# Performance work log

Hardware: AMD Instinct MI355X
Metric: run time of the kernel (lower is better)

## Reference

```python
import jax, jax.numpy as jnp
import numpy as np

D_MODEL = 1024
EXPAND = 2
D_INNER = D_MODEL * EXPAND  # 2048
D_STATE = 16
D_CONV = 4
DT_RANK = (D_MODEL + 15) // 16  # 64
BATCH = 2
SEQ = 1024


def setup_inputs() -> dict:
    key = jax.random.key(0)
    ks = jax.random.split(key, 10)
    s = lambda d: 1.0 / np.sqrt(d)
    x = jax.random.normal(ks[0], (BATCH, SEQ, D_MODEL), dtype=jnp.float32)
    W_in = jax.random.normal(ks[1], (D_MODEL, 2 * D_INNER), dtype=jnp.float32) * s(D_MODEL)
    conv_w = jax.random.normal(ks[2], (D_INNER, D_CONV), dtype=jnp.float32) * s(D_CONV)
    conv_b = jax.random.normal(ks[3], (D_INNER,), dtype=jnp.float32) * 0.02
    W_x = jax.random.normal(ks[4], (D_INNER, DT_RANK + 2 * D_STATE), dtype=jnp.float32) * s(D_INNER)
    W_dt = jax.random.normal(ks[5], (DT_RANK, D_INNER), dtype=jnp.float32) * s(DT_RANK)
    b_dt = jax.random.uniform(ks[6], (D_INNER,), dtype=jnp.float32, minval=-4.0, maxval=-2.0)
    # S4D-real init: A = -[1..d_state] per channel
    A_log = jnp.log(jnp.tile(jnp.arange(1, D_STATE + 1, dtype=jnp.float32), (D_INNER, 1)))
    D = jnp.ones((D_INNER,), dtype=jnp.float32)
    W_out = jax.random.normal(ks[7], (D_INNER, D_MODEL), dtype=jnp.float32) * s(D_INNER)
    return {"x": x, "W_in": W_in, "conv_w": conv_w, "conv_b": conv_b,
            "W_x": W_x, "W_dt": W_dt, "b_dt": b_dt, "A_log": A_log,
            "D": D, "W_out": W_out}


def _mamba_forward(x, W_in, conv_w, conv_b, W_x, W_dt, b_dt, A_log, D, W_out):
    B, L, _ = x.shape
    # input projection -> [B, L, 2*d_inner], split into u (conv branch) and z (gate)
    xz = jnp.einsum('bld,de->ble', x, W_in)
    u, z = jnp.split(xz, 2, axis=-1)  # each [B, L, d_inner]

    # causal depthwise conv over time
    u_c = jnp.transpose(u, (0, 2, 1))                      # [B, d_inner, L]
    u_c = jnp.pad(u_c, ((0, 0), (0, 0), (D_CONV - 1, 0)))  # left pad for causality
    kern = conv_w[:, None, :]                              # [d_inner, 1, d_conv]
    u_c = jax.lax.conv_general_dilated(
        u_c, kern, window_strides=(1,), padding='VALID',
        dimension_numbers=('NCH', 'OIH', 'NCH'),
        feature_group_count=D_INNER)
    u_c = u_c + conv_b[None, :, None]
    u_c = jax.nn.silu(jnp.transpose(u_c, (0, 2, 1)))       # [B, L, d_inner]

    # data-dependent SSM parameters
    x_dbl = jnp.einsum('bld,de->ble', u_c, W_x)            # [B, L, dt_rank+2*d_state]
    dt_lowrank = x_dbl[..., :DT_RANK]
    Bmat = x_dbl[..., DT_RANK:DT_RANK + D_STATE]           # [B, L, d_state]
    Cmat = x_dbl[..., DT_RANK + D_STATE:]                  # [B, L, d_state]
    dt = jax.nn.softplus(jnp.einsum('blr,rd->bld', dt_lowrank, W_dt) + b_dt)

    A = -jnp.exp(A_log)                                    # [d_inner, d_state]

    # selective scan over time: h' = exp(dt*A) h + dt*B*u ; y = <h, C>
    def step(h, inp):
        u_t, dt_t, B_t, C_t = inp                          # [B,d], [B,d], [B,n], [B,n]
        dA = jnp.exp(dt_t[..., None] * A)                  # [B, d_inner, d_state]
        dBu = (dt_t * u_t)[..., None] * B_t[:, None, :]    # [B, d_inner, d_state]
        h = dA * h + dBu
        y_t = jnp.einsum('bdn,bn->bd', h, C_t)
        return h, y_t

    h0 = jnp.zeros((B, D_INNER, D_STATE), dtype=x.dtype)
    seq = (jnp.swapaxes(u_c, 0, 1), jnp.swapaxes(dt, 0, 1),
           jnp.swapaxes(Bmat, 0, 1), jnp.swapaxes(Cmat, 0, 1))
    _, ys = jax.lax.scan(step, h0, seq)                    # ys: [L, B, d_inner]
    y = jnp.swapaxes(ys, 0, 1) + u_c * D                   # skip term
    y = y * jax.nn.silu(z)                                 # gate
    return jnp.einsum('bld,de->ble', y, W_out)             # [B, L, d_model]


def reference(x, W_in, conv_w, conv_b, W_x, W_dt, b_dt, A_log, D, W_out):
    return _mamba_forward(x, W_in, conv_w, conv_b, W_x, W_dt, b_dt, A_log, D, W_out)
```

## Files before the change

kernel.cpp:

```cpp
#include <hip/hip_runtime.h>
#include <hip/hip_bf16.h>


typedef __attribute__((ext_vector_type(8))) short bfrag;
typedef __attribute__((ext_vector_type(4))) float f32x4;

#define CF   32
#define CLEN 32

__device__ __forceinline__ unsigned short f2bf(float f) {
    unsigned int u = __float_as_uint(f);
    u += 0x7FFF + ((u >> 16) & 1);
    return (unsigned short)(u >> 16);
}
__device__ __forceinline__ float bf2f(unsigned short s) {
    return __uint_as_float((unsigned int)s << 16);
}

__device__ __forceinline__ void async_copy16(const unsigned short* g,
                                             unsigned short* l) {
    __builtin_amdgcn_global_load_lds(
        (const __attribute__((address_space(1))) void*)g,
        (__attribute__((address_space(3))) void*)l, 16, 0, 0);
}

template<int MT, int NT>
__global__ __launch_bounds__(256) void gemm_bf16_v2(
    const unsigned short* __restrict__ A,
    const unsigned short* __restrict__ BT,
    float* __restrict__ C,
    unsigned short* __restrict__ Cb0,
    unsigned short* __restrict__ Cb1,
    int K, int lda, int ldb, int ldc, int split,
    const float* __restrict__ bias)
{
    constexpr int FI  = MT / 32;
    constexpr int FJ  = NT / 32;
    constexpr int ACH = MT / 32;
    constexpr int BCH = NT / 32;
    __shared__ __align__(16) unsigned short sA[MT * 64];
    __shared__ __align__(16) unsigned short sB[NT * 64];

    const int tid  = threadIdx.x;
    const int wave = tid >> 6, lane = tid & 63;
    const int lm   = lane & 15;
    const int quad = lane >> 4;
    const int wrow = (wave >> 1) * (MT / 2);
    const int wcol = (wave & 1) * (NT / 2);
    const int bm = blockIdx.y * MT, bn = blockIdx.x * NT;

    const int lrow = lane >> 3;
    const int lkb  = (lane & 7) ^ lrow;

    f32x4 acc[FI][FJ];
    #pragma unroll
    for (int i = 0; i < FI; ++i)
        #pragma unroll
        for (int j = 0; j < FJ; ++j) {
            acc[i][j][0] = 0.f; acc[i][j][1] = 0.f;
            acc[i][j][2] = 0.f; acc[i][j][3] = 0.f;
        }

    for (int k0 = 0; k0 < K; k0 += 64) {
        #pragma unroll
        for (int c = 0; c < ACH; ++c) {
            const int chunk = wave * ACH + c;
            const int row = chunk * 8 + lrow;
            async_copy16(&A[(size_t)(bm + row) * lda + k0 + lkb * 8],
                         &sA[chunk * 512 + lane * 8]);
        }
        #pragma unroll
        for (int c = 0; c < BCH; ++c) {
            const int chunk = wave * BCH + c;
            const int row = chunk * 8 + lrow;
            async_copy16(&BT[(size_t)(bn + row) * ldb + k0 + lkb * 8],
                         &sB[chunk * 512 + lane * 8]);
        }
        __syncthreads();

        #pragma unroll
        for (int ks = 0; ks < 2; ++ks) {
            bfrag af[FI], bf[FJ];
            #pragma unroll
            for (int i = 0; i < FI; ++i) {
                const int row = wrow + i * 16 + lm;
                const int slot = (ks * 4 + quad) ^ (row & 7);
                af[i] = *(const bfrag*)&sA[row * 64 + slot * 8];
            }
            #pragma unroll
            for (int j = 0; j < FJ; ++j) {
                const int row = wcol + j * 16 + lm;
                const int slot = (ks * 4 + quad) ^ (row & 7);
                bf[j] = *(const bfrag*)&sB[row * 64 + slot * 8];
            }
            #pragma unroll
            for (int i = 0; i < FI; ++i)
                #pragma unroll
                for (int j = 0; j < FJ; ++j)
                    acc[i][j] = __builtin_amdgcn_mfma_f32_16x16x32_bf16(
                        af[i], bf[j], acc[i][j], 0, 0, 0);
        }
        __syncthreads();
    }

    #pragma unroll
    for (int i = 0; i < FI; ++i)
        #pragma unroll
        for (int j = 0; j < FJ; ++j) {
            const int col = bn + wcol + j * 16 + lm;
            #pragma unroll
            for (int r = 0; r < 4; ++r) {
                const int row = bm + wrow + i * 16 + quad * 4 + r;
                float v = acc[i][j][r];
                if (bias != nullptr) {
                    v += bias[col];
                    v = (v > 20.f) ? v : logf(1.f + expf(v));
                    Cb0[(size_t)row * ldc + col] = f2bf(v);
                } else if (split > 0) {
                    if (col < split) Cb0[(size_t)row * split + col] = f2bf(v);
                    else             Cb1[(size_t)row * split + (col - split)] = f2bf(v);
                } else {
                    C[(size_t)row * ldc + col] = v;
                }
            }
        }
}

__global__ __launch_bounds__(256) void prep_fused(
    const float* __restrict__ W_in, const float* __restrict__ W_out,
    const float* __restrict__ W_dt, const float* __restrict__ x,
    unsigned short* __restrict__ wbT, unsigned short* __restrict__ wobT,
    unsigned short* __restrict__ wdtT, unsigned short* __restrict__ xb)
{
    __shared__ float tile[32][33];
    const int bx = blockIdx.x;
    const int tid = threadIdx.x;

    const float* in; unsigned short* out; int rows, cols, jt, it;
    if (bx < 4096)      { in = W_in;  out = wbT;  rows = 1024; cols = 4096;
                          jt = bx & 127; it = bx >> 7; }
    else if (bx < 6144) { int t = bx - 4096; in = W_out; out = wobT;
                          rows = 2048; cols = 1024; jt = t & 31; it = t >> 5; }
    else if (bx < 6272) { int t = bx - 6144; in = W_dt;  out = wdtT;
                          rows = 64;   cols = 2048; jt = t & 63; it = t >> 6; }
    else {
        int i = ((bx - 6272) * 256 + tid) * 4;
        float4 v = *(const float4*)&x[i];
        ushort4 o;
        o.x = f2bf(v.x); o.y = f2bf(v.y); o.z = f2bf(v.z); o.w = f2bf(v.w);
        *(ushort4*)&xb[i] = o;
        return;
    }
    const int j0 = jt * 32, i0 = it * 32;
    const int tx = tid & 31, ty = tid >> 5;
    #pragma unroll
    for (int k = 0; k < 4; ++k)
        tile[ty + 8 * k][tx] = in[(size_t)(i0 + ty + 8 * k) * cols + j0 + tx];
    __syncthreads();
    #pragma unroll
    for (int k = 0; k < 4; ++k)
        out[(size_t)(j0 + ty + 8 * k) * rows + i0 + tx] = f2bf(tile[tx][ty + 8 * k]);
}

#define SK_KS 128
__global__ __launch_bounds__(256) void gemm_f32_splitk(
    const unsigned short* __restrict__ A,
    const float* __restrict__ B,
    float* __restrict__ part)
{
    __shared__ __align__(16) float As[16][64];
    __shared__ __align__(16) float Bs[16][96];

    const int tid = threadIdx.x;
    const int mtile = blockIdx.x >> 4;
    const int kslice = blockIdx.x & 15;
    const int bm = mtile * 64;
    const int kbase = kslice * SK_KS;

    const int am = tid >> 2;
    const int ak = (tid & 3) << 2;

    const int ty = tid >> 4, tx = tid & 15;
    const int rm = ty << 2;
    const int rn = tx * 6;

    float acc[4][6] = {};

    for (int k0 = 0; k0 < SK_KS; k0 += 16) {
        ushort4 av = *(const ushort4*)&A[(size_t)(bm + am) * 2048 + kbase + k0 + ak];
        As[ak + 0][am] = bf2f(av.x);
        As[ak + 1][am] = bf2f(av.y);
        As[ak + 2][am] = bf2f(av.z);
        As[ak + 3][am] = bf2f(av.w);
        for (int i = tid; i < 384; i += 256) {
            int br = i / 24, bc = (i % 24) << 2;
            *(float4*)&Bs[br][bc] = *(const float4*)&B[(size_t)(kbase + k0 + br) * 96 + bc];
        }
        __syncthreads();

        #pragma unroll
        for (int k = 0; k < 16; ++k) {
            float4 a = *(const float4*)&As[k][rm];
            float b[6];
            #pragma unroll
            for (int j = 0; j < 6; ++j) b[j] = Bs[k][rn + j];
            #pragma unroll
            for (int j = 0; j < 6; ++j) {
                acc[0][j] += a.x * b[j];
                acc[1][j] += a.y * b[j];
                acc[2][j] += a.z * b[j];
                acc[3][j] += a.w * b[j];
            }
        }
        __syncthreads();
    }

    float* pout = part + (size_t)kslice * 196608;
    #pragma unroll
    for (int i = 0; i < 4; ++i) {
        float* crow = pout + (size_t)(bm + rm + i) * 96 + rn;
        #pragma unroll
        for (int j = 0; j < 6; ++j)
            crow[j] = acc[i][j];
    }
}

__global__ __launch_bounds__(256) void reduce_splitk(
    const float* __restrict__ part, float* __restrict__ xdbl,
    unsigned short* __restrict__ dtl)
{
    int i = (blockIdx.x * 256 + threadIdx.x) * 4;
    float4 acc = {0.f, 0.f, 0.f, 0.f};
    #pragma unroll
    for (int s = 0; s < 16; ++s) {
        float4 v = *(const float4*)&part[(size_t)s * 196608 + i];
        acc.x += v.x; acc.y += v.y; acc.z += v.z; acc.w += v.w;
    }
    *(float4*)&xdbl[i] = acc;
    int row = i / 96, col = i % 96;
    if (col < 64) {
        ushort4 o;
        o.x = f2bf(acc.x); o.y = f2bf(acc.y);
        o.z = f2bf(acc.z); o.w = f2bf(acc.w);
        *(ushort4*)&dtl[(size_t)row * 64 + col] = o;
    }
}

__global__ __launch_bounds__(256) void conv_silu_kernel(
    const unsigned short* __restrict__ ub, const float* __restrict__ cw,
    const float* __restrict__ cb, unsigned short* __restrict__ uc)
{
    int idx = blockIdx.x * 256 + threadIdx.x;
    int d = idx & 2047;
    int r = idx >> 11;
    int l = r & 1023;

    float4 w4 = *(const float4*)(cw + 4 * d);
    float w[4] = { w4.x, w4.y, w4.z, w4.w };
    float acc = cb[d];
    const unsigned short* up = ub + (size_t)r * 2048 + d;
    if (l >= 3) {
        acc += w[0] * bf2f(up[-3 * 2048]) + w[1] * bf2f(up[-2 * 2048])
             + w[2] * bf2f(up[-1 * 2048]) + w[3] * bf2f(up[0]);
    } else {
        #pragma unroll
        for (int j = 0; j < 4; ++j) {
            int lj = l - 3 + j;
            if (lj >= 0) acc += w[j] * bf2f(up[(j - 3) * 2048]);
        }
    }
    float sig = 1.f / (1.f + expf(-acc));
    uc[idx] = f2bf(acc * sig);
}

__global__ __launch_bounds__(256) void scan_pass1(
    const unsigned short* __restrict__ uc,
    const unsigned short* __restrict__ dtb,
    const float* __restrict__ xdbl,
    const float* __restrict__ A_log,
    float* __restrict__ Hend,
    float* __restrict__ Sdt)
{
    __shared__ __align__(16) unsigned short su [CLEN][256];
    __shared__ __align__(16) unsigned short sdt[CLEN][256];
    __shared__ float sB[CLEN][16];
    const int tid = threadIdx.x;
    const int bx  = blockIdx.x;
    const int c   = bx & (CF - 1);
    const int g   = (bx >> 5) & 7;
    const int b   = bx >> 8;
    const int dbase = g * 256;
    const int d   = dbase + tid;
    const size_t rowbase = (size_t)b * 1024 + c * CLEN;

    #pragma unroll
    for (int q = 0; q < 4; ++q) {
        int i = q * 256 + tid;
        int row = i >> 5, off = (i & 31) * 8;
        size_t gaddr = (rowbase + row) * 2048 + dbase + off;
        *(float4*)&su [row][off] = *(const float4*)&uc [gaddr];
        *(float4*)&sdt[row][off] = *(const float4*)&dtb[gaddr];
    }
    for (int i = tid; i < CLEN * 16; i += 256) {
        int tt = i >> 4, nn = i & 15;
        sB[tt][nn] = xdbl[(rowbase + tt) * 96 + 64 + nn];
    }

    float A2[16];
    {
        float al[16];
        #pragma unroll
        for (int q = 0; q < 4; ++q)
            *(float4*)&al[4 * q] = *(const float4*)&A_log[(size_t)d * 16 + 4 * q];
        #pragma unroll
        for (int n = 0; n < 16; ++n) A2[n] = -expf(al[n]) * 1.44269504f;
    }
    __syncthreads();

    float h[16];
    #pragma unroll
    for (int n = 0; n < 16; ++n) h[n] = 0.f;
    float sdtv = 0.f;

    #pragma unroll 4
    for (int t = 0; t < CLEN; ++t) {
        float dtv = bf2f(sdt[t][tid]);
        float uv  = bf2f(su [t][tid]);
        sdtv += dtv;
        float dtu = dtv * uv;
        float bl[16];
        #pragma unroll
        for (int q = 0; q < 4; ++q)
            *(float4*)&bl[4 * q] = *(const float4*)&sB[t][4 * q];
        #pragma unroll
        for (int n = 0; n < 16; ++n)
            h[n] = exp2f(dtv * A2[n]) * h[n] + dtu * bl[n];
    }

    size_t base = ((size_t)(b * CF + c) * 2048 + d) * 16;
    #pragma unroll
    for (int q = 0; q < 4; ++q)
        *(float4*)&Hend[base + 4 * q] = *(float4*)&h[4 * q];
    Sdt[(size_t)(b * CF + c) * 2048 + d] = sdtv;
}

__global__ __launch_bounds__(256) void scan_pass2(
    const float* __restrict__ Hend, const float* __restrict__ Sdt,
    const float* __restrict__ A_log, float* __restrict__ Hin)
{
    int gid = blockIdx.x * 256 + threadIdx.x;
    int b = gid >> 15;
    int rest = gid & 32767;
    int d = rest >> 4;
    float A2 = -expf(A_log[rest]) * 1.44269504f;
    float H = 0.f;
    #pragma unroll
    for (int c = 0; c < CF; ++c) {
        size_t sidx = (size_t)(b * CF + c) * 2048 + d;
        size_t idx  = ((size_t)(b * CF + c) << 15) + rest;
        Hin[idx] = H;
        H = exp2f(A2 * Sdt[sidx]) * H + Hend[idx];
    }
}

__global__ __launch_bounds__(256) void scan_pass3(
    const unsigned short* __restrict__ uc,
    const unsigned short* __restrict__ dtb,
    const unsigned short* __restrict__ zb,
    const float* __restrict__ xdbl,
    const float* __restrict__ A_log,
    const float* __restrict__ Dvec,
    const float* __restrict__ Hin,
    unsigned short* __restrict__ yb)
{
    __shared__ __align__(16) unsigned short su [CLEN][256];
    __shared__ __align__(16) unsigned short sdt[CLEN][256];
    __shared__ __align__(16) unsigned short sz [CLEN][256];
    __shared__ float sBC[CLEN][32];
    const int tid = threadIdx.x;
    const int bx  = blockIdx.x;
    const int c   = bx & (CF - 1);
    const int g   = (bx >> 5) & 7;
    const int b   = bx >> 8;
    const int dbase = g * 256;
    const int d   = dbase + tid;
    const size_t rowbase = (size_t)b * 1024 + c * CLEN;

    #pragma unroll
    for (int q = 0; q < 4; ++q) {
        int i = q * 256 + tid;
        int row = i >> 5, off = (i & 31) * 8;
        size_t gaddr = (rowbase + row) * 2048 + dbase + off;
        *(float4*)&su [row][off] = *(const float4*)&uc [gaddr];
        *(float4*)&sdt[row][off] = *(const float4*)&dtb[gaddr];
        *(float4*)&sz [row][off] = *(const float4*)&zb [gaddr];
    }
    for (int i = tid; i < CLEN * 32; i += 256) {
        int tt = i >> 5, j = i & 31;
        sBC[tt][j] = xdbl[(rowbase + tt) * 96 + 64 + j];
    }

    float A2[16];
    {
        float al[16];
        #pragma unroll
        for (int q = 0; q < 4; ++q)
            *(float4*)&al[4 * q] = *(const float4*)&A_log[(size_t)d * 16 + 4 * q];
        #pragma unroll
        for (int n = 0; n < 16; ++n) A2[n] = -expf(al[n]) * 1.44269504f;
    }
    const float Dd = Dvec[d];

    float h[16];
    {
        size_t base = ((size_t)(b * CF + c) * 2048 + d) * 16;
        #pragma unroll
        for (int q = 0; q < 4; ++q)
            *(float4*)&h[4 * q] = *(const float4*)&Hin[base + 4 * q];
    }
    __syncthreads();

    #pragma unroll 4
    for (int t = 0; t < CLEN; ++t) {
        float dtv = bf2f(sdt[t][tid]);
        float uv  = bf2f(su [t][tid]);
        float zv  = bf2f(sz [t][tid]);
        float dtu = dtv * uv;
        float bl[16], cl[16];
        #pragma unroll
        for (int q = 0; q < 4; ++q) {
            *(float4*)&bl[4 * q] = *(const float4*)&sBC[t][4 * q];
            *(float4*)&cl[4 * q] = *(const float4*)&sBC[t][16 + 4 * q];
        }
        float acc = uv * Dd;
        #pragma unroll
        for (int n = 0; n < 16; ++n) {
            h[n] = exp2f(dtv * A2[n]) * h[n] + dtu * bl[n];
            acc += h[n] * cl[n];
        }
        float yv = acc * zv / (1.f + expf(-zv));
        sz[t][tid] = f2bf(yv);
    }
    __syncthreads();

    #pragma unroll
    for (int q = 0; q < 4; ++q) {
        int i = q * 256 + tid;
        int row = i >> 5, off = (i & 31) * 8;
        size_t gaddr = (rowbase + row) * 2048 + dbase + off;
        *(float4*)&yb[gaddr] = *(const float4*)&sz[row][off];
    }
}

extern "C" void kernel_launch(void* const* d_in, const int* in_sizes, int n_in,
                              void* d_out, int out_size, void* d_ws, size_t ws_size,
                              hipStream_t stream)
{
    const float* x      = (const float*)d_in[0];
    const float* W_in   = (const float*)d_in[1];
    const float* conv_w = (const float*)d_in[2];
    const float* conv_b = (const float*)d_in[3];
    const float* W_x    = (const float*)d_in[4];
    const float* W_dt   = (const float*)d_in[5];
    const float* b_dt   = (const float*)d_in[6];
    const float* A_log  = (const float*)d_in[7];
    const float* Dv     = (const float*)d_in[8];
    const float* W_out  = (const float*)d_in[9];
    float* out = (float*)d_out;

    float* ws = (float*)d_ws;
    unsigned short* ub  = (unsigned short*)ws;
    unsigned short* dtb = ub;
    unsigned short* uc  = ub + 4194304;
    float* xdbl = ws + 4194304;
    unsigned short* dtl = (unsigned short*)(xdbl + 196608);
    float* Hend = xdbl + 196608 + 65536;
    float* Hin  = Hend + 2097152;
    float* Sdt  = Hin + 2097152;
    float* part = Hend;
    unsigned short* zb   = (unsigned short*)(Sdt + 131072);
    unsigned short* xb   = zb + 4194304;
    unsigned short* wbT  = xb + 2097152;
    unsigned short* wobT = wbT + 4194304;
    unsigned short* wdtT = wobT + 2097152;
    unsigned short* yb   = wbT;

    dim3 blk(256);

    prep_fused<<<8320, blk, 0, stream>>>(W_in, W_out, W_dt, x,
                                         wbT, wobT, wdtT, xb);

    gemm_bf16_v2<128, 128><<<dim3(32, 16), blk, 0, stream>>>(
        xb, wbT, nullptr, ub, zb, 1024, 1024, 1024, 2048, 2048, nullptr);

    conv_silu_kernel<<<(2048 * 2048) / 256, blk, 0, stream>>>(ub, conv_w, conv_b, uc);

    gemm_f32_splitk<<<512, blk, 0, stream>>>(uc, W_x, part);
    reduce_splitk<<<192, blk, 0, stream>>>(part, xdbl, dtl);

    gemm_bf16_v2<128, 128><<<dim3(16, 16), blk, 0, stream>>>(
        dtl, wdtT, nullptr, dtb, nullptr, 64, 64, 64, 2048, 0, b_dt);

    scan_pass1<<<512, blk, 0, stream>>>(uc, dtb, xdbl, A_log, Hend, Sdt);
    scan_pass2<<<256, blk, 0, stream>>>(Hend, Sdt, A_log, Hin);
    scan_pass3<<<512, blk, 0, stream>>>(uc, dtb, zb, xdbl, A_log, Dv, Hin, yb);

    gemm_bf16_v2<64, 64><<<dim3(16, 32), blk, 0, stream>>>(
        yb, wobT, out, nullptr, nullptr, 2048, 2048, 2048, 1024, 0, nullptr);
}
```

Baseline: 269.4 us.

## Fuse dt projection and softplus into scan passes; vectorize conv-silu

Removes the standalone dt GEMM (K=64) and its 8 MB bf16 dt buffer. Each scan block now computes its own 32x256 dt tile with MFMA from the low-rank dtl and the transposed W_dt, applies bias and softplus, and writes the result to shared memory. Because pass1 and pass3 each do this, the dt GEMM runs twice, but one launch and a full write plus two reads of dt are saved. The conv-silu kernel also now handles 8 channels per thread with vector loads and stores.

```diff
diff --git a/kernel.cpp b/kernel.cpp
--- a/kernel.cpp
+++ b/kernel.cpp
@@ -31,8 +31,7 @@
     float* __restrict__ C,
     unsigned short* __restrict__ Cb0,
     unsigned short* __restrict__ Cb1,
-    int K, int lda, int ldb, int ldc, int split,
-    const float* __restrict__ bias)
+    int K, int lda, int ldb, int ldc, int split)
 {
     constexpr int FI  = MT / 32;
     constexpr int FJ  = NT / 32;
@@ -112,11 +111,7 @@
             for (int r = 0; r < 4; ++r) {
                 const int row = bm + wrow + i * 16 + quad * 4 + r;
                 float v = acc[i][j][r];
-                if (bias != nullptr) {
-                    v += bias[col];
-                    v = (v > 20.f) ? v : logf(1.f + expf(v));
-                    Cb0[(size_t)row * ldc + col] = f2bf(v);
-                } else if (split > 0) {
+                if (split > 0) {
                     if (col < split) Cb0[(size_t)row * split + col] = f2bf(v);
                     else             Cb1[(size_t)row * split + (col - split)] = f2bf(v);
                 } else {
@@ -251,38 +246,112 @@
     const float* __restrict__ cb, unsigned short* __restrict__ uc)
 {
     int idx = blockIdx.x * 256 + threadIdx.x;
-    int d = idx & 2047;
-    int r = idx >> 11;
-    int l = r & 1023;
-
-    float4 w4 = *(const float4*)(cw + 4 * d);
-    float w[4] = { w4.x, w4.y, w4.z, w4.w };
-    float acc = cb[d];
-    const unsigned short* up = ub + (size_t)r * 2048 + d;
-    if (l >= 3) {
-        acc += w[0] * bf2f(up[-3 * 2048]) + w[1] * bf2f(up[-2 * 2048])
-             + w[2] * bf2f(up[-1 * 2048]) + w[3] * bf2f(up[0]);
-    } else {
+    int r  = idx >> 8;
+    int d0 = (idx & 255) * 8;
+    int l  = r & 1023;
+
+    float4 w[8];
+    #pragma unroll
+    for (int q = 0; q < 8; ++q) w[q] = *(const float4*)&cw[(d0 + q) * 4];
+
+    float acc[8];
+    #pragma unroll
+    for (int q = 0; q < 8; ++q) acc[q] = cb[d0 + q];
+
+    const unsigned short* up = ub + (size_t)r * 2048 + d0;
+    #pragma unroll
+    for (int j = 0; j < 4; ++j) {
+        int lj = l - 3 + j;
+        if (lj >= 0) {
+            const unsigned short* rp = up + (ptrdiff_t)(j - 3) * 2048;
+            ushort4 a = *(const ushort4*)&rp[0];
+            ushort4 b4 = *(const ushort4*)&rp[4];
+            float uv[8] = { bf2f(a.x), bf2f(a.y), bf2f(a.z), bf2f(a.w),
+                            bf2f(b4.x), bf2f(b4.y), bf2f(b4.z), bf2f(b4.w) };
+            #pragma unroll
+            for (int q = 0; q < 8; ++q)
+                acc[q] += uv[q] * ((const float*)&w[q])[j];
+        }
+    }
+    ushort4 o0, o1;
+    float s;
+    s = 1.f / (1.f + expf(-acc[0])); o0.x = f2bf(acc[0] * s);
+    s = 1.f / (1.f + expf(-acc[1])); o0.y = f2bf(acc[1] * s);
+    s = 1.f / (1.f + expf(-acc[2])); o0.z = f2bf(acc[2] * s);
+    s = 1.f / (1.f + expf(-acc[3])); o0.w = f2bf(acc[3] * s);
+    s = 1.f / (1.f + expf(-acc[4])); o1.x = f2bf(acc[4] * s);
+    s = 1.f / (1.f + expf(-acc[5])); o1.y = f2bf(acc[5] * s);
+    s = 1.f / (1.f + expf(-acc[6])); o1.z = f2bf(acc[6] * s);
+    s = 1.f / (1.f + expf(-acc[7])); o1.w = f2bf(acc[7] * s);
+    *(ushort4*)&uc[(size_t)r * 2048 + d0]     = o0;
+    *(ushort4*)&uc[(size_t)r * 2048 + d0 + 4] = o1;
+}
+
+__device__ __forceinline__ void compute_dt_tile(
+    const unsigned short* __restrict__ wdtT, const float* __restrict__ b_dt,
+    const unsigned short (*sdtl)[72], unsigned short (*sdt)[256],
+    int dbase, int tid)
+{
+    const int wave = tid >> 6, lane = tid & 63;
+    const int lm = lane & 15, quad = lane >> 4;
+
+    f32x4 dacc[2][4];
+    #pragma unroll
+    for (int mi = 0; mi < 2; ++mi)
         #pragma unroll
         for (int j = 0; j < 4; ++j) {
-            int lj = l - 3 + j;
-            if (lj >= 0) acc += w[j] * bf2f(up[(j - 3) * 2048]);
-        }
-    }
-    float sig = 1.f / (1.f + expf(-acc));
-    uc[idx] = f2bf(acc * sig);
+            dacc[mi][j][0] = 0.f; dacc[mi][j][1] = 0.f;
+            dacc[mi][j][2] = 0.f; dacc[mi][j][3] = 0.f;
+        }
+
+    #pragma unroll
+    for (int kc = 0; kc < 2; ++kc) {
+        bfrag a[2], bw[4];
+        #pragma unroll
+        for (int mi = 0; mi < 2; ++mi)
+            a[mi] = *(const bfrag*)&sdtl[mi * 16 + lm][kc * 32 + quad * 8];
+        #pragma unroll
+        for (int j = 0; j < 4; ++j) {
+            const int dg = dbase + wave * 64 + j * 16 + lm;
+            bw[j] = *(const bfrag*)&wdtT[(size_t)dg * 64 + kc * 32 + quad * 8];
+        }
+        #pragma unroll
+        for (int mi = 0; mi < 2; ++mi)
+            #pragma unroll
+            for (int j = 0; j < 4; ++j)
+                dacc[mi][j] = __builtin_amdgcn_mfma_f32_16x16x32_bf16(
+                    a[mi], bw[j], dacc[mi][j], 0, 0, 0);
+    }
+
+    #pragma unroll
+    for (int j = 0; j < 4; ++j) {
+        const int dl = wave * 64 + j * 16 + lm;
+        const float bb = b_dt[dbase + dl];
+        #pragma unroll
+        for (int mi = 0; mi < 2; ++mi)
+            #pragma unroll
+            for (int r = 0; r < 4; ++r) {
+                const int t = mi * 16 + quad * 4 + r;
+                float v = dacc[mi][j][r] + bb;
+                v = (v > 20.f) ? v : logf(1.f + expf(v));
+                sdt[t][dl] = f2bf(v);
+            }
+    }
 }
 
 __global__ __launch_bounds__(256) void scan_pass1(
     const unsigned short* __restrict__ uc,
-    const unsigned short* __restrict__ dtb,
+    const unsigned short* __restrict__ dtl,
+    const unsigned short* __restrict__ wdtT,
+    const float* __restrict__ b_dt,
     const float* __restrict__ xdbl,
     const float* __restrict__ A_log,
     float* __restrict__ Hend,
     float* __restrict__ Sdt)
 {
-    __shared__ __align__(16) unsigned short su [CLEN][256];
-    __shared__ __align__(16) unsigned short sdt[CLEN][256];
+    __shared__ __align__(16) unsigned short su  [CLEN][256];
+    __shared__ __align__(16) unsigned short sdt [CLEN][256];
+    __shared__ __align__(16) unsigned short sdtl[CLEN][72];
     __shared__ float sB[CLEN][16];
     const int tid = threadIdx.x;
     const int bx  = blockIdx.x;
@@ -297,9 +366,13 @@
     for (int q = 0; q < 4; ++q) {
         int i = q * 256 + tid;
         int row = i >> 5, off = (i & 31) * 8;
-        size_t gaddr = (rowbase + row) * 2048 + dbase + off;
-        *(float4*)&su [row][off] = *(const float4*)&uc [gaddr];
-        *(float4*)&sdt[row][off] = *(const float4*)&dtb[gaddr];
+        *(float4*)&su[row][off] = *(const float4*)&uc[(rowbase + row) * 2048 + dbase + off];
+    }
+    #pragma unroll
+    for (int q = 0; q < 2; ++q) {
+        int i = q * 256 + tid;
+        int row = i >> 4, col = (i & 15) * 4;
+        *(ushort4*)&sdtl[row][col] = *(const ushort4*)&dtl[(rowbase + row) * 64 + col];
     }
     for (int i = tid; i < CLEN * 16; i += 256) {
         int tt = i >> 4, nn = i & 15;
@@ -315,6 +388,9 @@
         #pragma unroll
         for (int n = 0; n < 16; ++n) A2[n] = -expf(al[n]) * 1.44269504f;
     }
+    __syncthreads();
+
+    compute_dt_tile(wdtT, b_dt, sdtl, sdt, dbase, tid);
     __syncthreads();
 
     float h[16];
@@ -365,7 +441,9 @@
 
 __global__ __launch_bounds__(256) void scan_pass3(
     const unsigned short* __restrict__ uc,
-    const unsigned short* __restrict__ dtb,
+    const unsigned short* __restrict__ dtl,
+    const unsigned short* __restrict__ wdtT,
+    const float* __restrict__ b_dt,
     const unsigned short* __restrict__ zb,
     const float* __restrict__ xdbl,
     const float* __restrict__ A_log,
@@ -373,9 +451,10 @@
     const float* __restrict__ Hin,
     unsigned short* __restrict__ yb)
 {
-    __shared__ __align__(16) unsigned short su [CLEN][256];
-    __shared__ __align__(16) unsigned short sdt[CLEN][256];
-    __shared__ __align__(16) unsigned short sz [CLEN][256];
+    __shared__ __align__(16) unsigned short su  [CLEN][256];
+    __shared__ __align__(16) unsigned short sdt [CLEN][256];
+    __shared__ __align__(16) unsigned short sz  [CLEN][256];
+    __shared__ __align__(16) unsigned short sdtl[CLEN][72];
     __shared__ float sBC[CLEN][32];
     const int tid = threadIdx.x;
     const int bx  = blockIdx.x;
@@ -391,9 +470,14 @@
         int i = q * 256 + tid;
         int row = i >> 5, off = (i & 31) * 8;
         size_t gaddr = (rowbase + row) * 2048 + dbase + off;
-        *(float4*)&su [row][off] = *(const float4*)&uc [gaddr];
-        *(float4*)&sdt[row][off] = *(const float4*)&dtb[gaddr];
-        *(float4*)&sz [row][off] = *(const float4*)&zb [gaddr];
+        *(float4*)&su[row][off] = *(const float4*)&uc[gaddr];
+        *(float4*)&sz[row][off] = *(const float4*)&zb[gaddr];
+    }
+    #pragma unroll
+    for (int q = 0; q < 2; ++q) {
+        int i = q * 256 + tid;
+        int row = i >> 4, col = (i & 15) * 4;
+        *(ushort4*)&sdtl[row][col] = *(const ushort4*)&dtl[(rowbase + row) * 64 + col];
     }
     for (int i = tid; i < CLEN * 32; i += 256) {
         int tt = i >> 5, j = i & 31;
@@ -418,6 +502,9 @@
         for (int q = 0; q < 4; ++q)
             *(float4*)&h[4 * q] = *(const float4*)&Hin[base + 4 * q];
     }
+    __syncthreads();
+
+    compute_dt_tile(wdtT, b_dt, sdtl, sdt, dbase, tid);
     __syncthreads();
 
     #pragma unroll 4
@@ -470,7 +557,6 @@
 
     float* ws = (float*)d_ws;
     unsigned short* ub  = (unsigned short*)ws;
-    unsigned short* dtb = ub;
     unsigned short* uc  = ub + 4194304;
     float* xdbl = ws + 4194304;
     unsigned short* dtl = (unsigned short*)(xdbl + 196608);
@@ -491,20 +577,17 @@
                                          wbT, wobT, wdtT, xb);
 
     gemm_bf16_v2<128, 128><<<dim3(32, 16), blk, 0, stream>>>(
-        xb, wbT, nullptr, ub, zb, 1024, 1024, 1024, 2048, 2048, nullptr);
-
-    conv_silu_kernel<<<(2048 * 2048) / 256, blk, 0, stream>>>(ub, conv_w, conv_b, uc);
+        xb, wbT, nullptr, ub, zb, 1024, 1024, 1024, 2048, 2048);
+
+    conv_silu_kernel<<<2048, blk, 0, stream>>>(ub, conv_w, conv_b, uc);
 
     gemm_f32_splitk<<<512, blk, 0, stream>>>(uc, W_x, part);
     reduce_splitk<<<192, blk, 0, stream>>>(part, xdbl, dtl);
 
-    gemm_bf16_v2<128, 128><<<dim3(16, 16), blk, 0, stream>>>(
-        dtl, wdtT, nullptr, dtb, nullptr, 64, 64, 64, 2048, 0, b_dt);
-
-    scan_pass1<<<512, blk, 0, stream>>>(uc, dtb, xdbl, A_log, Hend, Sdt);
+    scan_pass1<<<512, blk, 0, stream>>>(uc, dtl, wdtT, b_dt, xdbl, A_log, Hend, Sdt);
     scan_pass2<<<256, blk, 0, stream>>>(Hend, Sdt, A_log, Hin);
-    scan_pass3<<<512, blk, 0, stream>>>(uc, dtb, zb, xdbl, A_log, Dv, Hin, yb);
+    scan_pass3<<<512, blk, 0, stream>>>(uc, dtl, wdtT, b_dt, zb, xdbl, A_log, Dv, Hin, yb);
 
     gemm_bf16_v2<64, 64><<<dim3(16, 32), blk, 0, stream>>>(
-        yb, wobT, out, nullptr, nullptr, 2048, 2048, 2048, 1024, 0, nullptr);
-}
+        yb, wobT, out, nullptr, nullptr, 2048, 2048, 2048, 1024, 0);
+}
```

Measured after the change: 259.6 us. -3.7%, faster.
